# Performance work log

Measured on AMD Instinct MI355X. Metric: run time of the kernel, lower is better.

## Reference

```python
import jax, jax.numpy as jnp
import numpy as np

I, H, O = 256, 512, 256  # input_size, hidden_size, output_size
B, S = 4096, 50


def _lstm_cell(x_t, h, c, Wih, Whh, bih, bhh):
    # torch gate order: i, f, g, o
    gates = x_t @ Wih.T + h @ Whh.T + bih + bhh  # [B, 4H]
    i, f, g, o = jnp.split(gates, 4, axis=-1)
    i = jax.nn.sigmoid(i)
    f = jax.nn.sigmoid(f)
    g = jnp.tanh(g)
    o = jax.nn.sigmoid(o)
    c_new = f * c + i * g
    h_new = o * jnp.tanh(c_new)
    return h_new, c_new


def setup_inputs() -> dict:
    key = jax.random.key(0)
    ks = jax.random.split(key, 12)
    s_i = 1.0 / np.sqrt(H)  # torch LSTM/Linear init scale
    u = lambda k, shape: jax.random.uniform(k, shape, jnp.float32, -s_i, s_i)
    return {
        "x": jax.random.normal(ks[0], (B, S, I), jnp.float32),
        "enc_Wih": u(ks[1], (4 * H, I)),
        "enc_Whh": u(ks[2], (4 * H, H)),
        "enc_bih": u(ks[3], (4 * H,)),
        "enc_bhh": u(ks[4], (4 * H,)),
        "dec_Wih": u(ks[5], (4 * H, I)),
        "dec_Whh": u(ks[6], (4 * H, H)),
        "dec_bih": u(ks[7], (4 * H,)),
        "dec_bhh": u(ks[8], (4 * H,)),
        "fc_W": u(ks[9], (O, H)),
        "fc_b": u(ks[10], (O,)),
        "target_seq_length": 20,
    }


def reference(x, enc_Wih, enc_Whh, enc_bih, enc_bhh,
              dec_Wih, dec_Whh, dec_bih, dec_bhh,
              fc_W, fc_b, target_seq_length):
    batch = x.shape[0]
    h0 = jnp.zeros((batch, H), x.dtype)
    c0 = jnp.zeros((batch, H), x.dtype)

    # ---- encoder: scan over time ----
    def enc_step(carry, x_t):
        h, c = carry
        h, c = _lstm_cell(x_t, h, c, enc_Wih, enc_Whh, enc_bih, enc_bhh)
        return (h, c), None

    (h, c), _ = jax.lax.scan(enc_step, (h0, c0), jnp.swapaxes(x, 0, 1))

    dec_in0 = jnp.zeros((batch, I), x.dtype)

    def dec_step(carry, _):
        h, c, inp = carry
        h, c = _lstm_cell(inp, h, c, dec_Wih, dec_Whh, dec_bih, dec_bhh)
        out = h @ fc_W.T + fc_b  # [B, O]
        return (h, c, out), out

    _, outs = jax.lax.scan(dec_step, (h, c, dec_in0), None,
                           length=target_seq_length)
    return jnp.swapaxes(outs, 0, 1)  # [B, T, O]
```

## Files before the change

kernel.cpp:

```cpp
#include <hip/hip_runtime.h>

#define I_SZ 256
#define H_SZ 512
#define O_SZ 256
#define B_SZ 4096
#define S_SZ 50
#define T_SZ 20
#define G4H  2048
#define BH   ((size_t)B_SZ * H_SZ)
#define NB   512

#define PAD 72
#define PAD_H 36

typedef _Float16 half8 __attribute__((ext_vector_type(8)));
typedef float f32x4 __attribute__((ext_vector_type(4)));

__device__ __forceinline__ float sigm(float x) {
    return 1.0f / (1.0f + __expf(-x));
}
__device__ __forceinline__ float tanh_fast(float x) {
    float e = __expf(2.0f * x);
    return 1.0f - 2.0f / (e + 1.0f);
}

#define GLDS(gp, lp) __builtin_amdgcn_global_load_lds(                      \
    (const __attribute__((address_space(1))) void*)(gp),                    \
    (__attribute__((address_space(3))) void*)(lp), 16, 0, 0)

#define MEMFENCE asm volatile("" ::: "memory")

__global__ void k_zeroN(unsigned* p, int n) {
    int i = blockIdx.x * blockDim.x + threadIdx.x;
    if (i < n) p[i] = 0u;
}

__global__ void k_cvt(const float* __restrict__ src, _Float16* __restrict__ dst, int n) {
    int i = blockIdx.x * blockDim.x + threadIdx.x;
    if (i < n) dst[i] = (_Float16)src[i];
}

__global__ void k_bias_combine(const float* __restrict__ a, const float* __restrict__ b,
                               float* __restrict__ dst, int n) {
    int i = blockIdx.x * blockDim.x + threadIdx.x;
    if (i < n) dst[i] = a[i] + b[i];
}

__global__ __launch_bounds__(256) void k_cvt_x(const float* __restrict__ x,
                                               _Float16* __restrict__ xT) {
    size_t idx = ((size_t)blockIdx.x * 256 + threadIdx.x) * 8;
    int i = (int)(idx & 255);
    int s = (int)((idx >> 8) % S_SZ);
    size_t b = idx / (256 * S_SZ);
    float4 v0 = *(const float4*)(x + idx);
    float4 v1 = *(const float4*)(x + idx + 4);
    half8 hv;
    hv[0] = (_Float16)v0.x; hv[1] = (_Float16)v0.y;
    hv[2] = (_Float16)v0.z; hv[3] = (_Float16)v0.w;
    hv[4] = (_Float16)v1.x; hv[5] = (_Float16)v1.y;
    hv[6] = (_Float16)v1.z; hv[7] = (_Float16)v1.w;
    *(half8*)(xT + (((size_t)s * B_SZ + b) * I_SZ + i)) = hv;
}

__global__ void k_wenc(const float* __restrict__ eWih, const float* __restrict__ eWhh,
                       _Float16* __restrict__ Wenc) {
    int idx = blockIdx.x * blockDim.x + threadIdx.x;
    int r = idx / 768, col = idx % 768;
    float v = (col < 256) ? eWih[(size_t)r * 256 + col] : eWhh[(size_t)r * 512 + col - 256];
    Wenc[idx] = (_Float16)v;
}

__global__ __launch_bounds__(256) void k_wd(
    const float* __restrict__ dWhh, const float* __restrict__ dWih,
    const float* __restrict__ fcW, _Float16* __restrict__ Wd)
{
    __shared__ float sA[8][256];
    const int tid = threadIdx.x;
    const int r0 = blockIdx.x * 8;
    {
        int linear = tid * 8;
        int row = linear >> 8, col = linear & 255;
        const float4* p = (const float4*)(dWih + (size_t)(r0 + row) * 256 + col);
        float4 v0 = p[0], v1 = p[1];
        *(float4*)&sA[row][col]     = v0;
        *(float4*)&sA[row][col + 4] = v1;
    }
    __syncthreads();
    float acc[8][2] = {};
    const int k = tid;
    for (int i = 0; i < 256; ++i) {
        float w0 = fcW[(size_t)i * 512 + k];
        float w1 = fcW[(size_t)i * 512 + k + 256];
        #pragma unroll
        for (int rr = 0; rr < 8; ++rr) {
            float a = sA[rr][i];
            acc[rr][0] += a * w0;
            acc[rr][1] += a * w1;
        }
    }
    #pragma unroll
    for (int rr = 0; rr < 8; ++rr) {
        size_t base = (size_t)(r0 + rr) * 512;
        Wd[base + k]       = (_Float16)(dWhh[base + k]       + acc[rr][0]);
        Wd[base + k + 256] = (_Float16)(dWhh[base + k + 256] + acc[rr][1]);
    }
}

__global__ __launch_bounds__(256) void k_bd(
    const float* __restrict__ dWih, const float* __restrict__ fcb,
    const float* __restrict__ db, float* __restrict__ bd)
{
    __shared__ float sf[256];
    const int tid = threadIdx.x;
    sf[tid] = fcb[tid];
    __syncthreads();
    int r = blockIdx.x * 256 + tid;
    float acc = db[r];
    const float* row = dWih + (size_t)r * 256;
    for (int o = 0; o < 256; o += 4) {
        float4 v = *(const float4*)(row + o);
        acc += v.x * sf[o] + v.y * sf[o + 1] + v.z * sf[o + 2] + v.w * sf[o + 3];
    }
    bd[r] = acc;
}

__global__ __launch_bounds__(256, 2) void k_lstm_all(
    const _Float16* __restrict__ xT,
    const _Float16* __restrict__ Wenc,
    const _Float16* __restrict__ dWhh_h,
    const _Float16* __restrict__ Wd,
    const float* __restrict__ eb, const float* __restrict__ db,
    const float* __restrict__ bd,
    _Float16* __restrict__ henc,
    _Float16* __restrict__ hseq,
    unsigned* __restrict__ bar)
{
    __shared__ _Float16 lds[2][2][128 * 64];

    const int tid = threadIdx.x;
    const int xcd = blockIdx.x & 7, slot = blockIdx.x >> 3;
    const int mb = (xcd >> 1) * 8 + (slot >> 3);
    const int jb = (xcd & 1) * 8 + (slot & 7);
    const int m0 = mb * 128, j0 = jb * 32;
    unsigned* grp = bar + mb * 16;

    const int wv = tid >> 6, lane = tid & 63, lrow = lane & 15, lk8 = (lane >> 4) * 8;
    const int wm = wv >> 1, wn = wv & 1;

    const int colb  = (lane & 7) * 16;
    const int scolh = (colb ^ (((lane >> 3) & 7) << 4)) >> 1;
    const _Float16* wEncQ[4]; const _Float16* wD0Q[4]; const _Float16* wDQ[4];
    const _Float16* xQ[4];
    unsigned aOffQ[4];
    int ldsQ[4];
    #pragma unroll
    for (int q = 0; q < 4; ++q) {
        int r = q * 32 + wv * 8 + (lane >> 3);
        int grow = ((r >> 4) & 3) * H_SZ + j0 + (r >> 6) * 16 + (r & 15);
        wEncQ[q] = Wenc   + (size_t)grow * 768 + scolh;
        wD0Q[q]  = dWhh_h + (size_t)grow * 512 + scolh;
        wDQ[q]   = Wd     + (size_t)grow * 512 + scolh;
        xQ[q]    = xT + (size_t)(m0 + r) * I_SZ + scolh;
        aOffQ[q] = (unsigned)((m0 + r) * H_SZ) + scolh;
        ldsQ[q]  = (q * 256 + wv * 64) * 8;
    }

    float ebj[4], dbj[4], bdj[4];
    #pragma unroll
    for (int nf = 0; nf < 4; ++nf) {
        int col = nf * H_SZ + j0 + wn * 16 + lrow;
        ebj[nf] = eb[col]; dbj[nf] = db[col]; bdj[nf] = bd[col];
    }

    float creg[4][4];

    auto wait_group = [&](unsigned target) {
        MEMFENCE;
        if (tid == 0) {
            while (__hip_atomic_load(grp, __ATOMIC_RELAXED, __HIP_MEMORY_SCOPE_AGENT) < target)
                __builtin_amdgcn_s_sleep(1);
        }
        __builtin_amdgcn_s_barrier();
        MEMFENCE;
    };
    auto arrive = [&]() {
        __syncthreads();
        if (tid == 0)
            __hip_atomic_fetch_add(grp, 1u, __ATOMIC_RELAXED, __HIP_MEMORY_SCOPE_AGENT);
    };

    auto compute = [&](int buf, f32x4 (&acc)[4][4]) {
        #pragma unroll
        for (int kc = 0; kc < 2; ++kc) {
            const int sc = (((kc * 32 + lk8) * 2) ^ ((lrow & 7) << 4)) >> 1;
            half8 a[4], b[4];
            #pragma unroll
            for (int mf = 0; mf < 4; ++mf)
                a[mf] = *(const half8*)&lds[buf][0][(wm * 64 + mf * 16 + lrow) * 64 + sc];
            #pragma unroll
            for (int nf = 0; nf < 4; ++nf)
                b[nf] = *(const half8*)&lds[buf][1][(wn * 64 + nf * 16 + lrow) * 64 + sc];
            #pragma unroll
            for (int mf = 0; mf < 4; ++mf)
                #pragma unroll
                for (int nf = 0; nf < 4; ++nf)
                    acc[mf][nf] = __builtin_amdgcn_mfma_f32_16x16x32_f16(a[mf], b[nf], acc[mf][nf], 0, 0, 0);
        }
    };

    auto epilogue = [&](f32x4 (&acc)[4][4], const float (&bj)[4], _Float16* hout, bool first) {
        _Float16* hsm = &lds[0][0][0];
        const int lc = wn * 16 + lrow;
        #pragma unroll
        for (int mf = 0; mf < 4; ++mf)
            #pragma unroll
            for (int r = 0; r < 4; ++r) {
                int lr = wm * 64 + mf * 16 + (lane >> 4) * 4 + r;
                float gi = acc[mf][0][r] + bj[0];
                float gf = acc[mf][1][r] + bj[1];
                float gg = acc[mf][2][r] + bj[2];
                float go = acc[mf][3][r] + bj[3];
                float cold = first ? 0.0f : creg[mf][r];
                float cn = sigm(gf) * cold + sigm(gi) * tanh_fast(gg);
                creg[mf][r] = cn;
                hsm[lr * PAD_H + lc] = (_Float16)(sigm(go) * tanh_fast(cn));
            }
        __syncthreads();
        int rr = tid >> 3, k = tid & 7;
        #pragma unroll
        for (int q = 0; q < 4; ++q) {
            int r = rr + q * 32;
            unsigned long long v = *(const unsigned long long*)&hsm[r * PAD_H + k * 4];
            unsigned long long* dst =
                (unsigned long long*)(hout + (size_t)(m0 + r) * H_SZ + j0) + k;
            __hip_atomic_store(dst, v, __ATOMIC_RELAXED, __HIP_MEMORY_SCOPE_AGENT);
        }
    };

    {
        f32x4 acc[4][4] = {};
        #pragma unroll
        for (int q = 0; q < 4; ++q) { GLDS(xQ[q], &lds[0][0][ldsQ[q]]); GLDS(wEncQ[q], &lds[0][1][ldsQ[q]]); }
        #pragma unroll
        for (int it = 0; it < 4; ++it) {
            if (it < 3) {
                #pragma unroll
                for (int q = 0; q < 4; ++q) {
                    GLDS(xQ[q] + (it + 1) * 64, &lds[(it + 1) & 1][0][ldsQ[q]]);
                    GLDS(wEncQ[q] + (it + 1) * 64, &lds[(it + 1) & 1][1][ldsQ[q]]);
                }
                asm volatile("s_waitcnt vmcnt(8)" ::: "memory");
            } else {
                asm volatile("s_waitcnt vmcnt(0)" ::: "memory");
            }
            __builtin_amdgcn_s_barrier(); MEMFENCE;
            compute(it & 1, acc);
            MEMFENCE; __builtin_amdgcn_s_barrier(); MEMFENCE;
        }
        epilogue(acc, ebj, henc, true);
        arrive();
    }

    for (int s = 1; s < S_SZ; ++s) {
        const size_t xoff = (size_t)s * B_SZ * I_SZ;
        const _Float16* hin = henc + (size_t)(s - 1) * BH;
        _Float16* hout = (s == S_SZ - 1) ? hseq : henc + (size_t)s * BH;
        f32x4 acc[4][4] = {};
        #pragma unroll
        for (int q = 0; q < 4; ++q) { GLDS(xQ[q] + xoff, &lds[0][0][ldsQ[q]]); GLDS(wEncQ[q], &lds[0][1][ldsQ[q]]); }
        #pragma unroll
        for (int it = 0; it < 12; ++it) {
            if (it < 11) {
                if (it == 3) wait_group((unsigned)s * 16u);
                #pragma unroll
                for (int q = 0; q < 4; ++q) {
                    if (it + 1 < 4) GLDS(xQ[q] + xoff + (it + 1) * 64, &lds[(it + 1) & 1][0][ldsQ[q]]);
                    else            GLDS(hin + aOffQ[q] + (it - 3) * 64, &lds[(it + 1) & 1][0][ldsQ[q]]);
                    GLDS(wEncQ[q] + (it + 1) * 64, &lds[(it + 1) & 1][1][ldsQ[q]]);
                }
                asm volatile("s_waitcnt vmcnt(8)" ::: "memory");
            } else {
                asm volatile("s_waitcnt vmcnt(0)" ::: "memory");
            }
            __builtin_amdgcn_s_barrier(); MEMFENCE;
            compute(it & 1, acc);
            MEMFENCE; __builtin_amdgcn_s_barrier(); MEMFENCE;
        }
        epilogue(acc, ebj, hout, false);
        arrive();
    }

    for (int t = 0; t < T_SZ; ++t) {
        const _Float16* hin = hseq + (size_t)t * BH;
        _Float16* hout = hseq + (size_t)(t + 1) * BH;
        const _Float16* wq[4];
        float bj[4];
        #pragma unroll
        for (int q = 0; q < 4; ++q) wq[q] = t ? wDQ[q] : wD0Q[q];
        #pragma unroll
        for (int nf = 0; nf < 4; ++nf) bj[nf] = t ? bdj[nf] : dbj[nf];

        wait_group((unsigned)(S_SZ + t) * 16u);
        f32x4 acc[4][4] = {};
        #pragma unroll
        for (int q = 0; q < 4; ++q) { GLDS(hin + aOffQ[q], &lds[0][0][ldsQ[q]]); GLDS(wq[q], &lds[0][1][ldsQ[q]]); }
        #pragma unroll
        for (int it = 0; it < 8; ++it) {
            if (it < 7) {
                #pragma unroll
                for (int q = 0; q < 4; ++q) {
                    GLDS(hin + aOffQ[q] + (it + 1) * 64, &lds[(it + 1) & 1][0][ldsQ[q]]);
                    GLDS(wq[q] + (it + 1) * 64, &lds[(it + 1) & 1][1][ldsQ[q]]);
                }
                asm volatile("s_waitcnt vmcnt(8)" ::: "memory");
            } else {
                asm volatile("s_waitcnt vmcnt(0)" ::: "memory");
            }
            __builtin_amdgcn_s_barrier(); MEMFENCE;
            compute(it & 1, acc);
            MEMFENCE; __builtin_amdgcn_s_barrier(); MEMFENCE;
        }
        epilogue(acc, bj, hout, false);
        if (t != T_SZ - 1) arrive();
    }
}

__global__ __launch_bounds__(256) void k_fc(
    const _Float16* __restrict__ hseq1,
    const _Float16* __restrict__ W,
    const float* __restrict__ bias,
    float* __restrict__ out)
{
    __shared__ _Float16 Asm[128][PAD];
    __shared__ _Float16 Bsm[128][PAD];

    const int tid = threadIdx.x;
    const int m0 = blockIdx.x * 128;
    const int t  = blockIdx.y;
    const int n0 = blockIdx.z * 128;
    const int wv = tid >> 6, lane = tid & 63, lrow = lane & 15, lk = (lane >> 4) * 8;
    const int wm = wv >> 1, wn = wv & 1;

    f32x4 acc[4][4] = {};

    const int srow = tid >> 3, skc = (tid & 7) * 8;
    const _Float16* A = hseq1 + (size_t)t * BH;

    for (int k0 = 0; k0 < H_SZ; k0 += 64) {
        __syncthreads();
        #pragma unroll
        for (int q = 0; q < 4; ++q) {
            int r = srow + q * 32;
            *(half8*)&Asm[r][skc] = *(const half8*)(A + (size_t)(m0 + r) * H_SZ + k0 + skc);
        }
        #pragma unroll
        for (int q = 0; q < 4; ++q) {
            int rr = srow + q * 32;
            *(half8*)&Bsm[rr][skc] = *(const half8*)(W + (size_t)(n0 + rr) * H_SZ + k0 + skc);
        }
        __syncthreads();
        #pragma unroll
        for (int kc = 0; kc < 64; kc += 32) {
            half8 a[4], b[4];
            #pragma unroll
            for (int mf = 0; mf < 4; ++mf) a[mf] = *(const half8*)&Asm[wm * 64 + mf * 16 + lrow][kc + lk];
            #pragma unroll
            for (int nf = 0; nf < 4; ++nf) b[nf] = *(const half8*)&Bsm[wn * 64 + nf * 16 + lrow][kc + lk];
            #pragma unroll
            for (int mf = 0; mf < 4; ++mf)
                #pragma unroll
                for (int nf = 0; nf < 4; ++nf)
                    acc[mf][nf] = __builtin_amdgcn_mfma_f32_16x16x32_f16(a[mf], b[nf], acc[mf][nf], 0, 0, 0);
        }
    }

    #pragma unroll
    for (int mf = 0; mf < 4; ++mf)
        #pragma unroll
        for (int nf = 0; nf < 4; ++nf) {
            int o = n0 + wn * 64 + nf * 16 + lrow;
            float bv = bias[o];
            #pragma unroll
            for (int r = 0; r < 4; ++r) {
                int m = m0 + wm * 64 + mf * 16 + (lane >> 4) * 4 + r;
                out[(size_t)m * (T_SZ * O_SZ) + (size_t)t * O_SZ + o] = acc[mf][nf][r] + bv;
            }
        }
}

extern "C" void kernel_launch(void* const* d_in, const int* in_sizes, int n_in,
                              void* d_out, int out_size, void* d_ws, size_t ws_size,
                              hipStream_t stream) {
    (void)in_sizes; (void)n_in; (void)out_size; (void)ws_size;

    const float* x    = (const float*)d_in[0];
    const float* eWih = (const float*)d_in[1];
    const float* eWhh = (const float*)d_in[2];
    const float* ebih = (const float*)d_in[3];
    const float* ebhh = (const float*)d_in[4];
    const float* dWih = (const float*)d_in[5];
    const float* dWhh = (const float*)d_in[6];
    const float* dbih = (const float*)d_in[7];
    const float* dbhh = (const float*)d_in[8];
    const float* fcW  = (const float*)d_in[9];
    const float* fcb  = (const float*)d_in[10];
    float* out = (float*)d_out;
    char* ws = (char*)d_ws;

    size_t off = 0;
    auto alloc = [&](size_t bytes) -> void* {
        void* p = ws + off;
        off += (bytes + 255) & ~(size_t)255;
        return p;
    };
    _Float16* xT     = (_Float16*)alloc((size_t)S_SZ * B_SZ * I_SZ * 2);
    _Float16* Wenc   = (_Float16*)alloc((size_t)G4H * (I_SZ + H_SZ) * 2);
    _Float16* dWhh_h = (_Float16*)alloc((size_t)G4H * H_SZ * 2);
    _Float16* Wd     = (_Float16*)alloc((size_t)G4H * H_SZ * 2);
    _Float16* fcW_h  = (_Float16*)alloc((size_t)O_SZ * H_SZ * 2);
    float*    eb     = (float*)alloc(G4H * 4);
    float*    db     = (float*)alloc(G4H * 4);
    float*    bd     = (float*)alloc(G4H * 4);
    _Float16* henc   = (_Float16*)alloc((size_t)(S_SZ - 1) * BH * 2);
    _Float16* hseq   = (_Float16*)alloc((size_t)(T_SZ + 1) * BH * 2);
    unsigned* bar    = (unsigned*)alloc(32 * 16 * 4);

    const int nWhh = G4H * H_SZ;
    const int nFc  = O_SZ * H_SZ;
    const size_t nX = (size_t)B_SZ * S_SZ * I_SZ;

    k_zeroN<<<2, 256, 0, stream>>>(bar, 32 * 16);
    k_cvt_x<<<(int)(nX / 8 / 256), 256, 0, stream>>>(x, xT);
    k_wenc<<<(G4H * 768) / 256, 256, 0, stream>>>(eWih, eWhh, Wenc);
    k_cvt<<<(nWhh + 255) / 256, 256, 0, stream>>>(dWhh, dWhh_h, nWhh);
    k_cvt<<<(nFc + 255) / 256, 256, 0, stream>>>(fcW, fcW_h, nFc);
    k_bias_combine<<<8, 256, 0, stream>>>(ebih, ebhh, eb, G4H);
    k_bias_combine<<<8, 256, 0, stream>>>(dbih, dbhh, db, G4H);
    k_wd<<<256, 256, 0, stream>>>(dWhh, dWih, fcW, Wd);
    k_bd<<<8, 256, 0, stream>>>(dWih, fcb, db, bd);

    k_lstm_all<<<NB, 256, 0, stream>>>(xT, Wenc, dWhh_h, Wd, eb, db, bd,
                                       henc, hseq, bar);

    k_fc<<<dim3(B_SZ / 128, T_SZ, O_SZ / 128), 256, 0, stream>>>(
        hseq + BH, fcW_h, fcb, out);
}
```

Baseline: 1.270 ms.

## Prefetch next step's first tiles in epilogue and restructure double-buffer barriers

Gives the h-staging tile its own LDS buffer so the epilogue no longer aliases the GEMM double buffer. The epilogue now issues the first weight and x tiles for the next timestep before signalling the group barrier. The K loop goes from two barriers per iteration to one, waiting on vmcnt(0) before issuing the next tile's loads. The goal is to hide the load latency at the start of each step behind the epilogue and the inter-block barrier, and to cut barrier count. The costs are extra LDS use, which may lower occupancy, and less overlap inside the K loop because it now waits for all outstanding loads.

Measured after the change: 1.702 ms. +34.1%, slower.

```diff
diff --git a/kernel.cpp b/kernel.cpp
--- a/kernel.cpp
+++ b/kernel.cpp
@@ -136,6 +136,7 @@
     unsigned* __restrict__ bar)
 {
     __shared__ _Float16 lds[2][2][128 * 64];
+    __shared__ _Float16 hsm[128 * PAD_H];
 
     const int tid = threadIdx.x;
     const int xcd = blockIdx.x & 7, slot = blockIdx.x >> 3;
@@ -183,11 +184,6 @@
         __builtin_amdgcn_s_barrier();
         MEMFENCE;
     };
-    auto arrive = [&]() {
-        __syncthreads();
-        if (tid == 0)
-            __hip_atomic_fetch_add(grp, 1u, __ATOMIC_RELAXED, __HIP_MEMORY_SCOPE_AGENT);
-    };
 
     auto compute = [&](int buf, f32x4 (&acc)[4][4]) {
         #pragma unroll
@@ -208,8 +204,10 @@
         }
     };
 
-    auto epilogue = [&](f32x4 (&acc)[4][4], const float (&bj)[4], _Float16* hout, bool first) {
-        _Float16* hsm = &lds[0][0][0];
+    auto epilogue = [&](f32x4 (&acc)[4][4], const float (&bj)[4], _Float16* hout,
+                        bool first, const _Float16* pfA, size_t pfAoff,
+                        const _Float16* const* pfBq, bool sig) {
+        MEMFENCE;
         const int lc = wn * 16 + lrow;
         #pragma unroll
         for (int mf = 0; mf < 4; ++mf)
@@ -225,16 +223,38 @@
                 creg[mf][r] = cn;
                 hsm[lr * PAD_H + lc] = (_Float16)(sigm(go) * tanh_fast(cn));
             }
-        __syncthreads();
-        int rr = tid >> 3, k = tid & 7;
-        #pragma unroll
-        for (int q = 0; q < 4; ++q) {
-            int r = rr + q * 32;
-            unsigned long long v = *(const unsigned long long*)&hsm[r * PAD_H + k * 4];
-            unsigned long long* dst =
-                (unsigned long long*)(hout + (size_t)(m0 + r) * H_SZ + j0) + k;
-            __hip_atomic_store(dst, v, __ATOMIC_RELAXED, __HIP_MEMORY_SCOPE_AGENT);
-        }
+        asm volatile("s_waitcnt lgkmcnt(0)" ::: "memory");
+        __builtin_amdgcn_s_barrier();
+        MEMFENCE;
+        {
+            int rr = tid >> 3, k = tid & 7;
+            #pragma unroll
+            for (int q = 0; q < 4; ++q) {
+                int r = rr + q * 32;
+                unsigned long long v = *(const unsigned long long*)&hsm[r * PAD_H + k * 4];
+                unsigned long long* dst =
+                    (unsigned long long*)(hout + (size_t)(m0 + r) * H_SZ + j0) + k;
+                __hip_atomic_store(dst, v, __ATOMIC_RELAXED, __HIP_MEMORY_SCOPE_AGENT);
+            }
+        }
+        int pf = 0;
+        if (pfBq) {
+            #pragma unroll
+            for (int q = 0; q < 4; ++q) GLDS(pfBq[q], &lds[0][1][ldsQ[q]]);
+            pf += 4;
+        }
+        if (pfA) {
+            #pragma unroll
+            for (int q = 0; q < 4; ++q) GLDS(pfA + pfAoff + (xQ[q] - xT), &lds[0][0][ldsQ[q]]);
+            pf += 4;
+        }
+        if (pf == 8)      { asm volatile("s_waitcnt vmcnt(8)" ::: "memory"); }
+        else if (pf == 4) { asm volatile("s_waitcnt vmcnt(4)" ::: "memory"); }
+        else              { asm volatile("s_waitcnt vmcnt(0)" ::: "memory"); }
+        __builtin_amdgcn_s_barrier();
+        MEMFENCE;
+        if (sig && tid == 0)
+            __hip_atomic_fetch_add(grp, 1u, __ATOMIC_RELAXED, __HIP_MEMORY_SCOPE_AGENT);
     };
 
     {
@@ -243,22 +263,18 @@
         for (int q = 0; q < 4; ++q) { GLDS(xQ[q], &lds[0][0][ldsQ[q]]); GLDS(wEncQ[q], &lds[0][1][ldsQ[q]]); }
         #pragma unroll
         for (int it = 0; it < 4; ++it) {
-            if (it < 3) {
+            asm volatile("s_waitcnt vmcnt(0)" ::: "memory");
+            __builtin_amdgcn_s_barrier(); MEMFENCE;
+            if (it + 1 < 4) {
                 #pragma unroll
                 for (int q = 0; q < 4; ++q) {
                     GLDS(xQ[q] + (it + 1) * 64, &lds[(it + 1) & 1][0][ldsQ[q]]);
                     GLDS(wEncQ[q] + (it + 1) * 64, &lds[(it + 1) & 1][1][ldsQ[q]]);
                 }
-                asm volatile("s_waitcnt vmcnt(8)" ::: "memory");
-            } else {
-                asm volatile("s_waitcnt vmcnt(0)" ::: "memory");
-            }
-            __builtin_amdgcn_s_barrier(); MEMFENCE;
-            compute(it & 1, acc);
-            MEMFENCE; __builtin_amdgcn_s_barrier(); MEMFENCE;
-        }
-        epilogue(acc, ebj, henc, true);
-        arrive();
+            }
+            compute(it & 1, acc); MEMFENCE;
+        }
+        epilogue(acc, ebj, henc, true, xT, (size_t)1 * B_SZ * I_SZ, wEncQ, true);
     }
 
     for (int s = 1; s < S_SZ; ++s) {
@@ -267,27 +283,24 @@
         _Float16* hout = (s == S_SZ - 1) ? hseq : henc + (size_t)s * BH;
         f32x4 acc[4][4] = {};
         #pragma unroll
-        for (int q = 0; q < 4; ++q) { GLDS(xQ[q] + xoff, &lds[0][0][ldsQ[q]]); GLDS(wEncQ[q], &lds[0][1][ldsQ[q]]); }
-        #pragma unroll
         for (int it = 0; it < 12; ++it) {
-            if (it < 11) {
-                if (it == 3) wait_group((unsigned)s * 16u);
+            asm volatile("s_waitcnt vmcnt(0)" ::: "memory");
+            if (it == 3) { wait_group((unsigned)s * 16u); }
+            else         { __builtin_amdgcn_s_barrier(); MEMFENCE; }
+            if (it + 1 < 12) {
                 #pragma unroll
                 for (int q = 0; q < 4; ++q) {
                     if (it + 1 < 4) GLDS(xQ[q] + xoff + (it + 1) * 64, &lds[(it + 1) & 1][0][ldsQ[q]]);
                     else            GLDS(hin + aOffQ[q] + (it - 3) * 64, &lds[(it + 1) & 1][0][ldsQ[q]]);
                     GLDS(wEncQ[q] + (it + 1) * 64, &lds[(it + 1) & 1][1][ldsQ[q]]);
                 }
-                asm volatile("s_waitcnt vmcnt(8)" ::: "memory");
-            } else {
-                asm volatile("s_waitcnt vmcnt(0)" ::: "memory");
-            }
-            __builtin_amdgcn_s_barrier(); MEMFENCE;
-            compute(it & 1, acc);
-            MEMFENCE; __builtin_amdgcn_s_barrier(); MEMFENCE;
-        }
-        epilogue(acc, ebj, hout, false);
-        arrive();
+            }
+            compute(it & 1, acc); MEMFENCE;
+        }
+        if (s < S_SZ - 1)
+            epilogue(acc, ebj, hout, false, xT, (size_t)(s + 1) * B_SZ * I_SZ, wEncQ, true);
+        else
+            epilogue(acc, ebj, hout, false, nullptr, 0, wD0Q, true);
     }
 
     for (int t = 0; t < T_SZ; ++t) {
@@ -303,25 +316,24 @@
         wait_group((unsigned)(S_SZ + t) * 16u);
         f32x4 acc[4][4] = {};
         #pragma unroll
-        for (int q = 0; q < 4; ++q) { GLDS(hin + aOffQ[q], &lds[0][0][ldsQ[q]]); GLDS(wq[q], &lds[0][1][ldsQ[q]]); }
+        for (int q = 0; q < 4; ++q) GLDS(hin + aOffQ[q], &lds[0][0][ldsQ[q]]);
         #pragma unroll
         for (int it = 0; it < 8; ++it) {
-            if (it < 7) {
+            asm volatile("s_waitcnt vmcnt(0)" ::: "memory");
+            __builtin_amdgcn_s_barrier(); MEMFENCE;
+            if (it + 1 < 8) {
                 #pragma unroll
                 for (int q = 0; q < 4; ++q) {
                     GLDS(hin + aOffQ[q] + (it + 1) * 64, &lds[(it + 1) & 1][0][ldsQ[q]]);
                     GLDS(wq[q] + (it + 1) * 64, &lds[(it + 1) & 1][1][ldsQ[q]]);
                 }
-                asm volatile("s_waitcnt vmcnt(8)" ::: "memory");
-            } else {
-                asm volatile("s_waitcnt vmcnt(0)" ::: "memory");
-            }
-            __builtin_amdgcn_s_barrier(); MEMFENCE;
-            compute(it & 1, acc);
-            MEMFENCE; __builtin_amdgcn_s_barrier(); MEMFENCE;
-        }
-        epilogue(acc, bj, hout, false);
-        if (t != T_SZ - 1) arrive();
+            }
+            compute(it & 1, acc); MEMFENCE;
+        }
+        if (t < T_SZ - 1)
+            epilogue(acc, bj, hout, false, nullptr, 0, wDQ, true);
+        else
+            epilogue(acc, bj, hout, false, nullptr, 0, nullptr, false);
     }
 }
 
```
